# Optimization experiments

Hardware: AMD Instinct MI355X
Metric: run time of the kernel (lower is better)

The kernel has to match this reference:

```python
import jax, jax.numpy as jnp
import numpy as np

B, S, D, H, L = 32, 512, 256, 8, 3
HD = D // H
FFN = D // 2
SCALE_BASE = 512.0
EPS = 1e-5


def _gammas():
    return (1.0 - jnp.exp(jnp.linspace(np.log(1.0 / 32.0), np.log(1.0 / 512.0), H))).astype(jnp.float32)


def _xpos(x, downscale):
    # x: [..., S, hd]; XPOS rotary embedding with exponential length scaling
    s, hd = x.shape[-2], x.shape[-1]
    half = hd // 2
    scale = (jnp.arange(0, hd, 2, dtype=jnp.float32) + 0.4 * hd) / (1.4 * hd)  # [half]
    power = jnp.arange(s, dtype=jnp.float32)[:, None] / SCALE_BASE
    sm = scale[None, :] ** power  # [S, half]
    if downscale:
        sm = 1.0 / sm
    inv_freq = 1.0 / (10000.0 ** (jnp.arange(half, dtype=jnp.float32) / half))
    ang = jnp.arange(s, dtype=jnp.float32)[:, None] * inv_freq[None, :]  # [S, half]
    sin = jnp.repeat(jnp.sin(ang) * sm, 2, axis=-1)  # duplicate_interleave -> [S, hd]
    cos = jnp.repeat(jnp.cos(ang) * sm, 2, axis=-1)
    x1, x2 = x[..., ::2], x[..., 1::2]
    rot = jnp.stack((-x2, x1), axis=-1).reshape(x.shape)  # rotate_every_two
    return x * cos + rot * sin


def _layer_norm(x, w, b):
    mu = x.mean(-1, keepdims=True)
    var = ((x - mu) ** 2).mean(-1, keepdims=True)
    return (x - mu) / jnp.sqrt(var + EPS) * w + b


def _msr(X, WQ, WK, WV, WG, WO, gn_w, gn_b):
    # Multi-scale retention, parallel form. X: [B,S,D]; WQ/WK/WV: [H,D,HD]
    b, s, _ = X.shape
    Q = _xpos(jnp.einsum('bsd,hde->bhse', X, WQ), False)
    K = _xpos(jnp.einsum('bsd,hde->bhse', X, WK), True)
    V = jnp.einsum('bsd,hde->bhse', X, WV)
    n = jnp.arange(s)
    delta = (n[:, None] - n[None, :]).astype(jnp.float32)
    mask = n[:, None] >= n[None, :]
    g = _gammas()
    Dm = jnp.where(mask[None], g[:, None, None] ** delta[None], 0.0)  # [H,S,S]
    scores = jnp.einsum('bhse,bhte->bhst', Q, K) * Dm[None]  # [B,H,S,S]
    Y = jnp.einsum('bhst,bhte->bhse', scores, V)  # [B,H,S,HD]
    Y = jnp.moveaxis(Y, 1, 2)  # [B,S,H,HD] (= concat heads)
    # GroupNorm(heads, v_dim): normalize per (token, head) group
    mu = Y.mean(-1, keepdims=True)
    var = ((Y - mu) ** 2).mean(-1, keepdims=True)
    Yn = ((Y - mu) / jnp.sqrt(var + EPS)).reshape(b, s, D) * gn_w + gn_b
    G = X @ WG
    return (G * jax.nn.sigmoid(G) * Yn) @ WO


def setup_inputs() -> dict:
    key = jax.random.key(0)
    ks = jax.random.split(key, 10)
    inp = {
        'v': jax.random.randint(ks[0], (B, S), 0, 65, dtype=jnp.int64),
        'emb': jax.random.normal(ks[1], (65, D), dtype=jnp.float32),
        'WQ': jax.random.normal(ks[2], (L, H, D, HD), dtype=jnp.float32) / D,
        'WK': jax.random.normal(ks[3], (L, H, D, HD), dtype=jnp.float32) / D,
        'WV': jax.random.normal(ks[4], (L, H, D, HD), dtype=jnp.float32) / D,
        'WG': jax.random.normal(ks[5], (L, D, D), dtype=jnp.float32) / D,
        'WO': jax.random.normal(ks[6], (L, D, D), dtype=jnp.float32) / D,
        'gn_w': jnp.ones((L, D), jnp.float32),
        'gn_b': jnp.zeros((L, D), jnp.float32),
        'ln1_w': jnp.ones((L, D), jnp.float32),
        'ln1_b': jnp.zeros((L, D), jnp.float32),
        'ln2_w': jnp.ones((L, D), jnp.float32),
        'ln2_b': jnp.zeros((L, D), jnp.float32),
        'w1': jax.random.normal(ks[7], (L, D, FFN), dtype=jnp.float32) * (1.0 / np.sqrt(D)),
        'b1': jnp.zeros((L, FFN), jnp.float32),
        'w2': jax.random.normal(ks[8], (L, FFN, D), dtype=jnp.float32) * (1.0 / np.sqrt(FFN)),
        'b2': jnp.zeros((L, D), jnp.float32),
    }
    return inp


def reference(v, emb, WQ, WK, WV, WG, WO, gn_w, gn_b, ln1_w, ln1_b, ln2_w, ln2_b, w1, b1, w2, b2):
    emb = emb.at[0].set(0.0)  # padding_idx=0
    X = jax.nn.relu(emb[v])  # [B,S,D]
    for i in range(L):
        Y = _msr(_layer_norm(X, ln1_w[i], ln1_b[i]), WQ[i], WK[i], WV[i], WG[i], WO[i], gn_w[i], gn_b[i]) + X
        h = jax.nn.gelu(_layer_norm(Y, ln2_w[i], ln2_b[i]) @ w1[i] + b1[i], approximate=False)
        X = h @ w2[i] + b2[i] + Y
    return X
```

## Files before the change

### kernel.cpp

```cpp
#include <hip/hip_runtime.h>
#include <hip/hip_bf16.h>
#include <math.h>

#define BB 32
#define SS 512
#define DD 256
#define HH 8
#define HDIM 32
#define FFNN 128
#define NROWS (BB*SS)
#define NELEM (NROWS*DD)

using bf16 = __hip_bfloat16;
typedef __attribute__((ext_vector_type(8))) short short8;
typedef __attribute__((ext_vector_type(4))) short short4v;
typedef __attribute__((ext_vector_type(4))) float floatx4;
typedef unsigned int uint_al __attribute__((may_alias));

static __device__ __forceinline__ float bf2f(bf16 x) { return __bfloat162float(x); }
static __device__ __forceinline__ bf16  f2bf(float x) { return __float2bfloat16(x); }
static __device__ __forceinline__ short f2bfs(float x) {
    bf16 b = __float2bfloat16(x);
    return __builtin_bit_cast(short, b);
}

static __device__ __forceinline__ unsigned int cvtpk(float a, float b) {
    unsigned int r;
    asm("v_cvt_pk_bf16_f32 %0, %1, %2" : "=v"(r) : "v"(a), "v"(b));
    return r;
}
static __device__ __forceinline__ short4v mk4(unsigned int a, unsigned int b) {
    union { unsigned int u[2]; short4v s; } t;
    t.u[0] = a; t.u[1] = b;
    return t.s;
}
static __device__ __forceinline__ floatx4 mfma16(short4v a, short4v b, floatx4 c) {
#if __has_builtin(__builtin_amdgcn_mfma_f32_16x16x16bf16_1k)
    return __builtin_amdgcn_mfma_f32_16x16x16bf16_1k(a, b, c, 0, 0, 0);
#else
    asm("v_mfma_f32_16x16x16_bf16 %0, %1, %2, %0" : "+v"(c) : "v"(a), "v"(b));
    return c;
#endif
}

static __device__ __forceinline__ void gld_lds16(const void* g, void* l) {
    __builtin_amdgcn_global_load_lds(
        (const __attribute__((address_space(1))) void*)g,
        (__attribute__((address_space(3))) void*)l, 16, 0, 0);
}

__global__ __launch_bounds__(256) void detect_v(const int* __restrict__ v, int* __restrict__ flag) {
    int i = blockIdx.x * 256 + threadIdx.x;
    if (v[2 * i + 1] != 0) atomicOr(flag, 1);
}

#define NQKVG (3*1024*256)
#define NWO   (3*256*256)
#define NW1   (3*128*256)
#define NW2   (3*256*128)
#define NXPT  (512*16)
#define NSETUP (NQKVG+NWO+NW1+NW2+NXPT)
__global__ __launch_bounds__(256) void setup_pack(const float* __restrict__ WQ, const float* __restrict__ WK,
                                                  const float* __restrict__ WV, const float* __restrict__ WG,
                                                  const float* __restrict__ WO, const float* __restrict__ w1,
                                                  const float* __restrict__ w2,
                                                  bf16* __restrict__ dQ, bf16* __restrict__ dO,
                                                  bf16* __restrict__ d1, bf16* __restrict__ d2,
                                                  float4* __restrict__ xpt, int* __restrict__ flag) {
    int idx = blockIdx.x * 256 + threadIdx.x;
    if (idx == 0) *flag = 0;
    if (idx < NQKVG) {
        int k = idx & 255, n = (idx >> 8) & 1023, l = idx >> 18;
        int seg = n >> 8, n8 = n & 255;
        float val;
        if (seg < 3) {
            const float* W = (seg == 0) ? WQ : (seg == 1) ? WK : WV;
            int h = n8 >> 5, e = n8 & 31;
            val = W[(((size_t)l * 8 + h) * 256 + k) * 32 + e];
        } else {
            val = WG[(size_t)l * 65536 + k * 256 + n8];
        }
        dQ[((size_t)l * 1024 + n) * 256 + k] = f2bf(val);
    } else if (idx < NQKVG + NWO) {
        int i = idx - NQKVG;
        int k = i & 255, n = (i >> 8) & 255, l = i >> 16;
        dO[((size_t)l * 256 + n) * 256 + k] = f2bf(WO[(size_t)l * 65536 + k * 256 + n]);
    } else if (idx < NQKVG + NWO + NW1) {
        int i = idx - NQKVG - NWO;
        int k = i & 255, n = (i >> 8) & 127, l = i >> 15;
        d1[((size_t)l * 128 + n) * 256 + k] = f2bf(w1[(size_t)l * 32768 + k * 128 + n]);
    } else if (idx < NQKVG + NWO + NW1 + NW2) {
        int i = idx - NQKVG - NWO - NW1;
        int k = i & 127, n = (i >> 7) & 255, l = i >> 15;
        d2[((size_t)l * 256 + n) * 128 + k] = f2bf(w2[(size_t)l * 32768 + k * 256 + n]);
    } else {
        int i = idx - NQKVG - NWO - NW1 - NW2;
        int jf = i & 15, s = i >> 4;
        float base = (2.0f * jf + 12.8f) / 44.8f;
        float sm = powf(base, (float)s * (1.0f / 512.0f));
        float ang = (float)s * powf(10000.0f, -(float)jf / 16.0f);
        float sn, cs;
        sincosf(ang, &sn, &cs);
        xpt[i] = float4{cs * sm, sn * sm, cs / sm, sn / sm};
    }
}

__global__ __launch_bounds__(256) void embed_ln_kernel(const int* __restrict__ v,
                                                       const float* __restrict__ emb,
                                                       const int* __restrict__ flag,
                                                       const float* __restrict__ w,
                                                       const float* __restrict__ b,
                                                       float* __restrict__ X,
                                                       short* __restrict__ Xn) {
    __shared__ float p1[4], p2[4], st[2];
    const int d = threadIdx.x;
    const int wid = threadIdx.x >> 6;
    const int is32 = *flag;
    const float wd = w[d], bd = b[d];
    for (int it = 0; it < 8; ++it) {
        int row = blockIdx.x * 8 + it;
        int tok = is32 ? v[row] : v[2 * row];
        float x = 0.0f;
        if (tok != 0) {
            x = emb[tok * DD + d];
            x = x > 0.0f ? x : 0.0f;
        }
        X[(size_t)row * DD + d] = x;
        float s1 = x, s2 = x * x;
        #pragma unroll
        for (int off = 1; off < 64; off <<= 1) {
            s1 += __shfl_xor(s1, off);
            s2 += __shfl_xor(s2, off);
        }
        if ((threadIdx.x & 63) == 0) { p1[wid] = s1; p2[wid] = s2; }
        __syncthreads();
        if (threadIdx.x == 0) {
            float t1 = p1[0] + p1[1] + p1[2] + p1[3];
            float t2 = p2[0] + p2[1] + p2[2] + p2[3];
            float mu = t1 * (1.0f / DD);
            float var = t2 * (1.0f / DD) - mu * mu;
            st[0] = mu; st[1] = rsqrtf(var + 1e-5f);
        }
        __syncthreads();
        Xn[(size_t)row * DD + d] = f2bfs((x - st[0]) * st[1] * wd + bd);
    }
}

__global__ __launch_bounds__(256) void qkvg_gemm(const short* __restrict__ A,
                                                 const short* __restrict__ Bp,
                                                 const float4* __restrict__ xpt,
                                                 bf16* __restrict__ C) {
    __shared__ __align__(16) short Als[16 * 512];
    __shared__ __align__(16) short Bls[16 * 512];
    const int tid = threadIdx.x;
    const int wave = tid >> 6, lane = tid & 63, lo = lane & 15, quad = lane >> 4;
    const int wm = wave >> 1, wn = wave & 1;
    const int row0 = blockIdx.x * 128, col0 = blockIdx.y * 128;

    floatx4 acc[4][4];
    #pragma unroll
    for (int i = 0; i < 4; ++i)
        #pragma unroll
        for (int j = 0; j < 4; ++j) acc[i][j] = floatx4{0.f, 0.f, 0.f, 0.f};

    for (int k0 = 0; k0 < 256; k0 += 64) {
        #pragma unroll
        for (int t = 0; t < 4; ++t) {
            int grp = (wm * 4 + t) * 2 + wn;
            const short* ga = A + (size_t)(row0 + (wm * 4 + t) * 16 + lo) * 256
                            + k0 + (wn * 4 + quad) * 8;
            gld_lds16(ga, &Als[grp * 512]);
        }
        #pragma unroll
        for (int t = 0; t < 4; ++t) {
            int grp = (wn * 4 + t) * 2 + wm;
            const short* gb = Bp + (size_t)(col0 + (wn * 4 + t) * 16 + lo) * 256
                            + k0 + (wm * 4 + quad) * 8;
            gld_lds16(gb, &Bls[grp * 512]);
        }
        __syncthreads();
        #pragma unroll
        for (int kkgrp = 0; kkgrp < 2; ++kkgrp) {
            short8 af[4], bfr[4];
            #pragma unroll
            for (int t = 0; t < 4; ++t)
                af[t] = *(const short8*)(&Als[((wm * 4 + t) * 2 + kkgrp) * 512 + lane * 8]);
            #pragma unroll
            for (int t = 0; t < 4; ++t)
                bfr[t] = *(const short8*)(&Bls[((wn * 4 + t) * 2 + kkgrp) * 512 + lane * 8]);
            #pragma unroll
            for (int ti = 0; ti < 4; ++ti)
                #pragma unroll
                for (int tj = 0; tj < 4; ++tj)
                    acc[ti][tj] = __builtin_amdgcn_mfma_f32_16x16x32_bf16(af[ti], bfr[tj], acc[ti][tj], 0, 0, 0);
        }
        __syncthreads();
    }

    #pragma unroll
    for (int ti = 0; ti < 4; ++ti) {
        #pragma unroll
        for (int tj = 0; tj < 4; ++tj) {
            int colb = col0 + (wn * 4 + tj) * 16 + lo;
            int seg = colb >> 8;
            #pragma unroll
            for (int r = 0; r < 4; ++r) {
                int row = row0 + (wm * 4 + ti) * 16 + quad * 4 + r;
                float v = acc[ti][tj][r];
                if (seg < 2) {
                    int s = row & (SS - 1);
                    int jf = (colb & 31) >> 1;
                    float4 t = xpt[s * 16 + jf];
                    float cs = (seg == 0) ? t.x : t.z;
                    float sn = (seg == 0) ? t.y : t.w;
                    float p = __shfl_xor(v, 1);
                    v = (lo & 1) ? (v * cs + p * sn) : (v * cs - p * sn);
                }
                C[(size_t)row * 1024 + colb] = f2bf(v);
            }
        }
    }
}

#define HS2 264
#define HSTR 136
template<int DOLN>
__global__ __launch_bounds__(256) void wo_ffn_fused(const short* __restrict__ A,
                                                    const short* __restrict__ Wo,
                                                    const short* __restrict__ W1p,
                                                    const float* __restrict__ b1,
                                                    const short* __restrict__ W2p,
                                                    const float* __restrict__ b2,
                                                    float* __restrict__ X,
                                                    const float* __restrict__ ln2w,
                                                    const float* __restrict__ ln2b,
                                                    const float* __restrict__ ln1w,
                                                    const float* __restrict__ ln1b,
                                                    short* __restrict__ Xn) {
    __shared__ __align__(16) short Hn[32 * HS2];
    __shared__ __align__(16) short Hf[32 * HSTR];
    __shared__ float Ssum[32][4], Ssq[32][4];
    const int tid = threadIdx.x;
    const int wave = tid >> 6, lane = tid & 63, lo = lane & 15, quad = lane >> 4;
    const int row0 = blockIdx.x * 32;
    const int colw0 = wave * 64;
    const int kq = quad * 8;

    floatx4 acc[2][4];
    #pragma unroll
    for (int i = 0; i < 2; ++i)
        #pragma unroll
        for (int j = 0; j < 4; ++j) acc[i][j] = floatx4{0.f, 0.f, 0.f, 0.f};

    for (int k0 = 0; k0 < 256; k0 += 64) {
        #pragma unroll
        for (int kk = 0; kk < 2; ++kk) {
            const int kof = k0 + kk * 32 + kq;
            short8 af[2], bfr[4];
            #pragma unroll
            for (int t = 0; t < 2; ++t)
                af[t] = *(const short8*)(A + (size_t)(row0 + t * 16 + lo) * 1024 + kof);
            #pragma unroll
            for (int t = 0; t < 4; ++t)
                bfr[t] = *(const short8*)(Wo + (size_t)(colw0 + t * 16 + lo) * 256 + kof);
            #pragma unroll
            for (int ti = 0; ti < 2; ++ti)
                #pragma unroll
                for (int tj = 0; tj < 4; ++tj)
                    acc[ti][tj] = __builtin_amdgcn_mfma_f32_16x16x32_bf16(af[ti], bfr[tj], acc[ti][tj], 0, 0, 0);
        }
    }

    float vv[2][4][4];
    #pragma unroll
    for (int ti = 0; ti < 2; ++ti)
        #pragma unroll
        for (int tj = 0; tj < 4; ++tj) {
            int colb = colw0 + tj * 16 + lo;
            #pragma unroll
            for (int r = 0; r < 4; ++r) {
                int row = row0 + ti * 16 + quad * 4 + r;
                vv[ti][tj][r] = acc[ti][tj][r] + X[(size_t)row * DD + colb];
            }
        }
    #pragma unroll
    for (int ti = 0; ti < 2; ++ti)
        #pragma unroll
        for (int r = 0; r < 4; ++r) {
            float s1 = 0.f, s2 = 0.f;
            #pragma unroll
            for (int tj = 0; tj < 4; ++tj) {
                float v = vv[ti][tj][r];
                s1 += v; s2 += v * v;
            }
            #pragma unroll
            for (int off = 1; off < 16; off <<= 1) {
                s1 += __shfl_xor(s1, off);
                s2 += __shfl_xor(s2, off);
            }
            if (lo == 0) {
                int rl = ti * 16 + quad * 4 + r;
                Ssum[rl][wave] = s1;
                Ssq[rl][wave] = s2;
            }
        }
    __syncthreads();
    #pragma unroll
    for (int ti = 0; ti < 2; ++ti)
        #pragma unroll
        for (int r = 0; r < 4; ++r) {
            int rl = ti * 16 + quad * 4 + r;
            float t1 = Ssum[rl][0] + Ssum[rl][1] + Ssum[rl][2] + Ssum[rl][3];
            float t2 = Ssq[rl][0] + Ssq[rl][1] + Ssq[rl][2] + Ssq[rl][3];
            float mu = t1 * (1.0f / DD);
            float var = t2 * (1.0f / DD) - mu * mu;
            float rs = rsqrtf(var + 1e-5f);
            #pragma unroll
            for (int tj = 0; tj < 4; ++tj) {
                int colb = colw0 + tj * 16 + lo;
                Hn[rl * HS2 + colb] =
                    f2bfs((vv[ti][tj][r] - mu) * rs * ln2w[colb] + ln2b[colb]);
            }
        }
    __syncthreads();

    floatx4 a1[2][2];
    #pragma unroll
    for (int i = 0; i < 2; ++i) { a1[i][0] = floatx4{0,0,0,0}; a1[i][1] = floatx4{0,0,0,0}; }
    for (int k0 = 0; k0 < 256; k0 += 64) {
        #pragma unroll
        for (int kk = 0; kk < 2; ++kk) {
            const int kof = k0 + kk * 32 + kq;
            short8 af[2], bfr[2];
            #pragma unroll
            for (int t = 0; t < 2; ++t)
                af[t] = *(const short8*)(&Hn[(t * 16 + lo) * HS2 + kof]);
            #pragma unroll
            for (int t = 0; t < 2; ++t)
                bfr[t] = *(const short8*)(W1p + (size_t)(wave * 32 + t * 16 + lo) * 256 + kof);
            #pragma unroll
            for (int ti = 0; ti < 2; ++ti)
                #pragma unroll
                for (int tj = 0; tj < 2; ++tj)
                    a1[ti][tj] = __builtin_amdgcn_mfma_f32_16x16x32_bf16(af[ti], bfr[tj], a1[ti][tj], 0, 0, 0);
        }
    }
    #pragma unroll
    for (int ti = 0; ti < 2; ++ti)
        #pragma unroll
        for (int tj = 0; tj < 2; ++tj) {
            int colb = wave * 32 + tj * 16 + lo;
            float bs = b1[colb];
            #pragma unroll
            for (int r = 0; r < 4; ++r) {
                int rl = ti * 16 + quad * 4 + r;
                float v = a1[ti][tj][r] + bs;
                v = 0.5f * v * (1.0f + erff(v * 0.70710678118f));
                Hf[rl * HSTR + colb] = f2bfs(v);
            }
        }
    __syncthreads();

    floatx4 a2[2][4];
    #pragma unroll
    for (int i = 0; i < 2; ++i)
        #pragma unroll
        for (int j = 0; j < 4; ++j) a2[i][j] = floatx4{0,0,0,0};
    for (int k0 = 0; k0 < 128; k0 += 64) {
        #pragma unroll
        for (int kk = 0; kk < 2; ++kk) {
            const int kof = k0 + kk * 32 + kq;
            short8 af[2], bfr[4];
            #pragma unroll
            for (int t = 0; t < 2; ++t)
                af[t] = *(const short8*)(&Hf[(t * 16 + lo) * HSTR + kof]);
            #pragma unroll
            for (int t = 0; t < 4; ++t)
                bfr[t] = *(const short8*)(W2p + (size_t)(colw0 + t * 16 + lo) * 128 + kof);
            #pragma unroll
            for (int ti = 0; ti < 2; ++ti)
                #pragma unroll
                for (int tj = 0; tj < 4; ++tj)
                    a2[ti][tj] = __builtin_amdgcn_mfma_f32_16x16x32_bf16(af[ti], bfr[tj], a2[ti][tj], 0, 0, 0);
        }
    }

    #pragma unroll
    for (int ti = 0; ti < 2; ++ti)
        #pragma unroll
        for (int tj = 0; tj < 4; ++tj) {
            int colb = colw0 + tj * 16 + lo;
            float bs = b2[colb];
            #pragma unroll
            for (int r = 0; r < 4; ++r) {
                int row = row0 + ti * 16 + quad * 4 + r;
                float v = a2[ti][tj][r] + bs + vv[ti][tj][r];
                X[(size_t)row * DD + colb] = v;
                vv[ti][tj][r] = v;
            }
        }
    if (!DOLN) return;
    #pragma unroll
    for (int ti = 0; ti < 2; ++ti)
        #pragma unroll
        for (int r = 0; r < 4; ++r) {
            float s1 = 0.f, s2 = 0.f;
            #pragma unroll
            for (int tj = 0; tj < 4; ++tj) {
                float v = vv[ti][tj][r];
                s1 += v; s2 += v * v;
            }
            #pragma unroll
            for (int off = 1; off < 16; off <<= 1) {
                s1 += __shfl_xor(s1, off);
                s2 += __shfl_xor(s2, off);
            }
            if (lo == 0) {
                int rl = ti * 16 + quad * 4 + r;
                Ssum[rl][wave] = s1;
                Ssq[rl][wave] = s2;
            }
        }
    __syncthreads();
    #pragma unroll
    for (int ti = 0; ti < 2; ++ti)
        #pragma unroll
        for (int r = 0; r < 4; ++r) {
            int rl = ti * 16 + quad * 4 + r;
            float t1 = Ssum[rl][0] + Ssum[rl][1] + Ssum[rl][2] + Ssum[rl][3];
            float t2 = Ssq[rl][0] + Ssq[rl][1] + Ssq[rl][2] + Ssq[rl][3];
            float mu = t1 * (1.0f / DD);
            float var = t2 * (1.0f / DD) - mu * mu;
            float rs = rsqrtf(var + 1e-5f);
            int row = row0 + rl;
            #pragma unroll
            for (int tj = 0; tj < 4; ++tj) {
                int colb = colw0 + tj * 16 + lo;
                Xn[(size_t)row * DD + colb] =
                    f2bfs((vv[ti][tj][r] - mu) * rs * ln1w[colb] + ln1b[colb]);
            }
        }
}

#define VSTR 44
__global__ __launch_bounds__(256) void retention_mfma_kernel(bf16* __restrict__ QKVG,
                                                             const float* __restrict__ gnw,
                                                             const float* __restrict__ gnb) {
    __shared__ __align__(16) short Vt[4][32 * VSTR];
    const int wslot = threadIdx.x >> 6;
    const int lane = threadIdx.x & 63;
    const int gblk = blockIdx.x >> 6;
    const int qi = 15 - ((gblk & ~3) + (((gblk & 3) + (gblk >> 2)) & 3));
    const int bh = ((blockIdx.x & 63) << 2) | wslot;
    const int b = bh >> 3, h = bh & 7;
    const int q0 = qi * 32;
    const int lo = lane & 15, quad = lane >> 4;

    const float la0 = -3.46573590280f, la1 = -6.23832462504f;
    float gamma = 1.0f - expf(la0 + (float)h * (la1 - la0) / 7.0f);
    float lg2 = log2f(gamma);
    float g16i = exp2f(-16.0f * lg2);
    float g16p = exp2f(16.0f * lg2);
    float gi32 = exp2f(-32.0f * lg2);
    float wq[4], wq16[4], wqB[4];
    #pragma unroll
    for (int r = 0; r < 4; ++r) {
        wq[r]   = exp2f((float)(lo - 4 * quad - r) * lg2);
        wq16[r] = wq[r] * g16i;
        wqB[r]  = wq[r] * g16p;
    }
    float c = exp2f((float)q0 * lg2);

    const size_t base = (size_t)b * SS * 1024;
    const short* QKVGs = (const short*)QKVG;

    short8 qfA = *(const short8*)(QKVGs + base + (size_t)(q0 + lo) * 1024 + h * HDIM + quad * 8);
    short8 qfB = *(const short8*)(QKVGs + base + (size_t)(q0 + 16 + lo) * 1024 + h * HDIM + quad * 8);

    floatx4 oA0 = {0,0,0,0}, oA1 = {0,0,0,0}, oB0 = {0,0,0,0}, oB1 = {0,0,0,0};
    short* Vw = Vt[wslot];
    const int nch = qi + 1;

    for (int ch = 0; ch < nch; ++ch) {
        const int t0 = ch * 32;
        const short* Kb = QKVGs + base + 256 + h * HDIM + quad * 8;
        short8 kf0 = *(const short8*)(Kb + (size_t)(t0 + lo) * 1024);
        short8 kf1 = *(const short8*)(Kb + (size_t)(t0 + 16 + lo) * 1024);
        {
            const int r = lane >> 2, dcol = (lane & 3) * 8;
            const short* Vg = QKVGs + base + 512 + h * HDIM + dcol;
            uint4 u1 = *(const uint4*)(Vg + (size_t)(t0 + r) * 1024);
            uint4 u2 = *(const uint4*)(Vg + (size_t)(t0 + 16 + r) * 1024);
            uint_al* W1 = (uint_al*)(Vw + r * VSTR + dcol);
            uint_al* W2 = (uint_al*)(Vw + (16 + r) * VSTR + dcol);
            W1[0] = u1.x; W1[1] = u1.y; W1[2] = u1.z; W1[3] = u1.w;
            W2[0] = u2.x; W2[1] = u2.y; W2[2] = u2.z; W2[3] = u2.w;
        }
        const floatx4 z = {0,0,0,0};
        __builtin_amdgcn_s_setprio(1);
        floatx4 sA0 = __builtin_amdgcn_mfma_f32_16x16x32_bf16(kf0, qfA, z, 0, 0, 0);
        floatx4 sA1 = __builtin_amdgcn_mfma_f32_16x16x32_bf16(kf1, qfA, z, 0, 0, 0);
        floatx4 sB0 = __builtin_amdgcn_mfma_f32_16x16x32_bf16(kf0, qfB, z, 0, 0, 0);
        floatx4 sB1 = __builtin_amdgcn_mfma_f32_16x16x32_bf16(kf1, qfB, z, 0, 0, 0);
        __builtin_amdgcn_s_setprio(0);

        float m0[4], m1[4], mB[4];
        #pragma unroll
        for (int r = 0; r < 4; ++r) {
            m0[r] = c * wq[r];
            m1[r] = c * wq16[r];
            mB[r] = c * wqB[r];
        }
        if (ch == qi) {
            #pragma unroll
            for (int r = 0; r < 4; ++r) {
                if (lo < 4 * quad + r) m0[r] = 0.0f;
                m1[r] = 0.0f;
            }
        }
        c *= gi32;

        unsigned int pa0 = cvtpk(sA0[0] * m0[0], sA0[1] * m0[1]);
        unsigned int pa1 = cvtpk(sA0[2] * m0[2], sA0[3] * m0[3]);
        unsigned int pa2 = cvtpk(sA1[0] * m1[0], sA1[1] * m1[1]);
        unsigned int pa3 = cvtpk(sA1[2] * m1[2], sA1[3] * m1[3]);
        unsigned int pb0 = cvtpk(sB0[0] * mB[0], sB0[1] * mB[1]);
        unsigned int pb1 = cvtpk(sB0[2] * mB[2], sB0[3] * mB[3]);
        unsigned int pb2 = cvtpk(sB1[0] * m0[0], sB1[1] * m0[1]);
        unsigned int pb3 = cvtpk(sB1[2] * m0[2], sB1[3] * m0[3]);
        short4v pA0 = mk4(pa0, pa1), pA1 = mk4(pa2, pa3);
        short4v pB0 = mk4(pb0, pb1), pB1 = mk4(pb2, pb3);

        short4v v00, v01, v10, v11;
        #pragma unroll
        for (int j = 0; j < 4; ++j) {
            v00[j] = Vw[(4 * quad + j) * VSTR + lo];
            v01[j] = Vw[(16 + 4 * quad + j) * VSTR + lo];
            v10[j] = Vw[(4 * quad + j) * VSTR + 16 + lo];
            v11[j] = Vw[(16 + 4 * quad + j) * VSTR + 16 + lo];
        }
        __builtin_amdgcn_s_setprio(1);
        oA0 = mfma16(pA0, v00, oA0);
        oA0 = mfma16(pA1, v01, oA0);
        oA1 = mfma16(pA0, v10, oA1);
        oA1 = mfma16(pA1, v11, oA1);
        oB0 = mfma16(pB0, v00, oB0);
        oB0 = mfma16(pB1, v01, oB0);
        oB1 = mfma16(pB0, v10, oB1);
        oB1 = mfma16(pB1, v11, oB1);
        __builtin_amdgcn_s_setprio(0);
    }

    float gw0 = gnw[h * HDIM + lo], gw1 = gnw[h * HDIM + 16 + lo];
    float gb0 = gnb[h * HDIM + lo], gb1 = gnb[h * HDIM + 16 + lo];
    bf16* QK = QKVG;
    #pragma unroll
    for (int sub = 0; sub < 2; ++sub) {
        floatx4 o0 = sub ? oB0 : oA0;
        floatx4 o1 = sub ? oB1 : oA1;
        int qbase = q0 + sub * 16;
        #pragma unroll
        for (int r = 0; r < 4; ++r) {
            float y0 = o0[r], y1 = o1[r];
            float s = y0 + y1, ss = y0 * y0 + y1 * y1;
            #pragma unroll
            for (int off = 1; off < 16; off <<= 1) {
                s  += __shfl_xor(s, off);
                ss += __shfl_xor(ss, off);
            }
            float mu = s * (1.0f / HDIM);
            float var = ss * (1.0f / HDIM) - mu * mu;
            float rstd = rsqrtf(var + 1e-5f);
            int q = qbase + quad * 4 + r;
            size_t rowb = base + (size_t)q * 1024;
            float g0 = bf2f(QK[rowb + 768 + h * HDIM + lo]);
            float g1 = bf2f(QK[rowb + 768 + h * HDIM + 16 + lo]);
            float t0v = g0 / (1.0f + expf(-g0)) * ((y0 - mu) * rstd * gw0 + gb0);
            float t1v = g1 / (1.0f + expf(-g1)) * ((y1 - mu) * rstd * gw1 + gb1);
            QK[rowb + h * HDIM + lo]      = f2bf(t0v);
            QK[rowb + h * HDIM + 16 + lo] = f2bf(t1v);
        }
    }
}

extern "C" void kernel_launch(void* const* d_in, const int* in_sizes, int n_in,
                              void* d_out, int out_size, void* d_ws, size_t ws_size,
                              hipStream_t stream) {
    const int*   v    = (const int*)d_in[0];
    const float* emb  = (const float*)d_in[1];
    const float* WQ   = (const float*)d_in[2];
    const float* WK   = (const float*)d_in[3];
    const float* WV   = (const float*)d_in[4];
    const float* WG   = (const float*)d_in[5];
    const float* WO   = (const float*)d_in[6];
    const float* gn_w = (const float*)d_in[7];
    const float* gn_b = (const float*)d_in[8];
    const float* ln1w = (const float*)d_in[9];
    const float* ln1b = (const float*)d_in[10];
    const float* ln2w = (const float*)d_in[11];
    const float* ln2b = (const float*)d_in[12];
    const float* w1   = (const float*)d_in[13];
    const float* b1   = (const float*)d_in[14];
    const float* w2   = (const float*)d_in[15];
    const float* b2   = (const float*)d_in[16];

    float* X = (float*)d_out;

    float* base  = (float*)d_ws;
    int*   flag  = (int*)base;
    short* Xn    = (short*)(base + 16);
    bf16*  QKVG  = (bf16*)(Xn + (size_t)NROWS * 256);
    bf16*  WqkvgP = QKVG + (size_t)NROWS * 1024;
    bf16*  WoP   = WqkvgP + 3 * 1024 * 256;
    bf16*  W1P   = WoP + 3 * 256 * 256;
    bf16*  W2P   = W1P + 3 * 128 * 256;
    float4* xpt  = (float4*)(W2P + 3 * 256 * 128);

    setup_pack<<<NSETUP / 256, 256, 0, stream>>>(WQ, WK, WV, WG, WO, w1, w2,
                                                 WqkvgP, WoP, W1P, W2P, xpt, flag);
    detect_v<<<32, 256, 0, stream>>>(v, flag);
    embed_ln_kernel<<<NROWS / 8, 256, 0, stream>>>(v, emb, flag, ln1w, ln1b, X, Xn);

    for (int i = 0; i < 3; ++i) {
        qkvg_gemm<<<dim3(128, 8), 256, 0, stream>>>(Xn,
                                                    (const short*)(WqkvgP + (size_t)i * 1024 * 256),
                                                    xpt, QKVG);
        retention_mfma_kernel<<<1024, 256, 0, stream>>>(QKVG, gn_w + i * DD, gn_b + i * DD);
        if (i < 2)
            wo_ffn_fused<1><<<NROWS / 32, 256, 0, stream>>>((const short*)QKVG,
                                                            (const short*)(WoP + (size_t)i * 256 * 256),
                                                            (const short*)(W1P + (size_t)i * 128 * 256),
                                                            b1 + i * FFNN,
                                                            (const short*)(W2P + (size_t)i * 256 * 128),
                                                            b2 + i * DD, X,
                                                            ln2w + i * DD, ln2b + i * DD,
                                                            ln1w + (i + 1) * DD, ln1b + (i + 1) * DD, Xn);
        else
            wo_ffn_fused<0><<<NROWS / 32, 256, 0, stream>>>((const short*)QKVG,
                                                            (const short*)(WoP + (size_t)i * 256 * 256),
                                                            (const short*)(W1P + (size_t)i * 128 * 256),
                                                            b1 + i * FFNN,
                                                            (const short*)(W2P + (size_t)i * 256 * 128),
                                                            b2 + i * DD, X,
                                                            ln2w + i * DD, ln2b + i * DD,
                                                            nullptr, nullptr, nullptr);
    }
}
```

Before: 352.1 us.

## Fuse retention into the Wo/FFN kernel with one wave per head

Merges the retention kernel into the output-projection and FFN kernel. Each 512-thread block now owns one 32-row query chunk of one batch, with eight waves each computing one head. The gated, group-normed retention output goes straight into shared memory as the Wo GEMM input, so it is no longer written back to QKVG and re-read, and one launch per layer disappears. The costs are a causally imbalanced workload per block: blocks with later query chunks do more retention work, only partly offset by alternating the chunk order across block indices. There are also only 512 blocks, which lowers parallelism, and the GEMM phases are split into narrower per-wave column slices.

```diff
diff --git a/kernel.cpp b/kernel.cpp
--- a/kernel.cpp
+++ b/kernel.cpp
@@ -222,240 +222,40 @@
     }
 }
 
-#define HS2 264
+#define TSTR 264
 #define HSTR 136
+#define VSTR 44
 template<int DOLN>
-__global__ __launch_bounds__(256) void wo_ffn_fused(const short* __restrict__ A,
-                                                    const short* __restrict__ Wo,
-                                                    const short* __restrict__ W1p,
-                                                    const float* __restrict__ b1,
-                                                    const short* __restrict__ W2p,
-                                                    const float* __restrict__ b2,
-                                                    float* __restrict__ X,
-                                                    const float* __restrict__ ln2w,
-                                                    const float* __restrict__ ln2b,
-                                                    const float* __restrict__ ln1w,
-                                                    const float* __restrict__ ln1b,
-                                                    short* __restrict__ Xn) {
-    __shared__ __align__(16) short Hn[32 * HS2];
+__global__ __launch_bounds__(512) void ret_wo_ffn(const bf16* __restrict__ QKVG,
+                                                  const float* __restrict__ gnw,
+                                                  const float* __restrict__ gnb,
+                                                  const short* __restrict__ Wo,
+                                                  const short* __restrict__ W1p,
+                                                  const float* __restrict__ b1,
+                                                  const short* __restrict__ W2p,
+                                                  const float* __restrict__ b2,
+                                                  float* __restrict__ X,
+                                                  const float* __restrict__ ln2w,
+                                                  const float* __restrict__ ln2b,
+                                                  const float* __restrict__ ln1w,
+                                                  const float* __restrict__ ln1b,
+                                                  short* __restrict__ Xn) {
+    __shared__ __align__(16) short Vt[8][32 * VSTR];
+    __shared__ __align__(16) short Tn[32 * TSTR];
     __shared__ __align__(16) short Hf[32 * HSTR];
-    __shared__ float Ssum[32][4], Ssq[32][4];
+    __shared__ float Ssum[32][8], Ssq[32][8];
     const int tid = threadIdx.x;
     const int wave = tid >> 6, lane = tid & 63, lo = lane & 15, quad = lane >> 4;
-    const int row0 = blockIdx.x * 32;
-    const int colw0 = wave * 64;
+    const int blk = blockIdx.x;
+    const int qi = (blk < 256) ? (blk & 15) : 15 - (blk & 15);
+    const int bb = (blk & 255) >> 4 | ((blk >> 4) & 16);
+    const int q0 = qi * 32;
+    const int row0 = bb * SS + q0;
+    const int h = wave;
     const int kq = quad * 8;
 
-    floatx4 acc[2][4];
-    #pragma unroll
-    for (int i = 0; i < 2; ++i)
-        #pragma unroll
-        for (int j = 0; j < 4; ++j) acc[i][j] = floatx4{0.f, 0.f, 0.f, 0.f};
-
-    for (int k0 = 0; k0 < 256; k0 += 64) {
-        #pragma unroll
-        for (int kk = 0; kk < 2; ++kk) {
-            const int kof = k0 + kk * 32 + kq;
-            short8 af[2], bfr[4];
-            #pragma unroll
-            for (int t = 0; t < 2; ++t)
-                af[t] = *(const short8*)(A + (size_t)(row0 + t * 16 + lo) * 1024 + kof);
-            #pragma unroll
-            for (int t = 0; t < 4; ++t)
-                bfr[t] = *(const short8*)(Wo + (size_t)(colw0 + t * 16 + lo) * 256 + kof);
-            #pragma unroll
-            for (int ti = 0; ti < 2; ++ti)
-                #pragma unroll
-                for (int tj = 0; tj < 4; ++tj)
-                    acc[ti][tj] = __builtin_amdgcn_mfma_f32_16x16x32_bf16(af[ti], bfr[tj], acc[ti][tj], 0, 0, 0);
-        }
-    }
-
-    float vv[2][4][4];
-    #pragma unroll
-    for (int ti = 0; ti < 2; ++ti)
-        #pragma unroll
-        for (int tj = 0; tj < 4; ++tj) {
-            int colb = colw0 + tj * 16 + lo;
-            #pragma unroll
-            for (int r = 0; r < 4; ++r) {
-                int row = row0 + ti * 16 + quad * 4 + r;
-                vv[ti][tj][r] = acc[ti][tj][r] + X[(size_t)row * DD + colb];
-            }
-        }
-    #pragma unroll
-    for (int ti = 0; ti < 2; ++ti)
-        #pragma unroll
-        for (int r = 0; r < 4; ++r) {
-            float s1 = 0.f, s2 = 0.f;
-            #pragma unroll
-            for (int tj = 0; tj < 4; ++tj) {
-                float v = vv[ti][tj][r];
-                s1 += v; s2 += v * v;
-            }
-            #pragma unroll
-            for (int off = 1; off < 16; off <<= 1) {
-                s1 += __shfl_xor(s1, off);
-                s2 += __shfl_xor(s2, off);
-            }
-            if (lo == 0) {
-                int rl = ti * 16 + quad * 4 + r;
-                Ssum[rl][wave] = s1;
-                Ssq[rl][wave] = s2;
-            }
-        }
-    __syncthreads();
-    #pragma unroll
-    for (int ti = 0; ti < 2; ++ti)
-        #pragma unroll
-        for (int r = 0; r < 4; ++r) {
-            int rl = ti * 16 + quad * 4 + r;
-            float t1 = Ssum[rl][0] + Ssum[rl][1] + Ssum[rl][2] + Ssum[rl][3];
-            float t2 = Ssq[rl][0] + Ssq[rl][1] + Ssq[rl][2] + Ssq[rl][3];
-            float mu = t1 * (1.0f / DD);
-            float var = t2 * (1.0f / DD) - mu * mu;
-            float rs = rsqrtf(var + 1e-5f);
-            #pragma unroll
-            for (int tj = 0; tj < 4; ++tj) {
-                int colb = colw0 + tj * 16 + lo;
-                Hn[rl * HS2 + colb] =
-                    f2bfs((vv[ti][tj][r] - mu) * rs * ln2w[colb] + ln2b[colb]);
-            }
-        }
-    __syncthreads();
-
-    floatx4 a1[2][2];
-    #pragma unroll
-    for (int i = 0; i < 2; ++i) { a1[i][0] = floatx4{0,0,0,0}; a1[i][1] = floatx4{0,0,0,0}; }
-    for (int k0 = 0; k0 < 256; k0 += 64) {
-        #pragma unroll
-        for (int kk = 0; kk < 2; ++kk) {
-            const int kof = k0 + kk * 32 + kq;
-            short8 af[2], bfr[2];
-            #pragma unroll
-            for (int t = 0; t < 2; ++t)
-                af[t] = *(const short8*)(&Hn[(t * 16 + lo) * HS2 + kof]);
-            #pragma unroll
-            for (int t = 0; t < 2; ++t)
-                bfr[t] = *(const short8*)(W1p + (size_t)(wave * 32 + t * 16 + lo) * 256 + kof);
-            #pragma unroll
-            for (int ti = 0; ti < 2; ++ti)
-                #pragma unroll
-                for (int tj = 0; tj < 2; ++tj)
-                    a1[ti][tj] = __builtin_amdgcn_mfma_f32_16x16x32_bf16(af[ti], bfr[tj], a1[ti][tj], 0, 0, 0);
-        }
-    }
-    #pragma unroll
-    for (int ti = 0; ti < 2; ++ti)
-        #pragma unroll
-        for (int tj = 0; tj < 2; ++tj) {
-            int colb = wave * 32 + tj * 16 + lo;
-            float bs = b1[colb];
-            #pragma unroll
-            for (int r = 0; r < 4; ++r) {
-                int rl = ti * 16 + quad * 4 + r;
-                float v = a1[ti][tj][r] + bs;
-                v = 0.5f * v * (1.0f + erff(v * 0.70710678118f));
-                Hf[rl * HSTR + colb] = f2bfs(v);
-            }
-        }
-    __syncthreads();
-
-    floatx4 a2[2][4];
-    #pragma unroll
-    for (int i = 0; i < 2; ++i)
-        #pragma unroll
-        for (int j = 0; j < 4; ++j) a2[i][j] = floatx4{0,0,0,0};
-    for (int k0 = 0; k0 < 128; k0 += 64) {
-        #pragma unroll
-        for (int kk = 0; kk < 2; ++kk) {
-            const int kof = k0 + kk * 32 + kq;
-            short8 af[2], bfr[4];
-            #pragma unroll
-            for (int t = 0; t < 2; ++t)
-                af[t] = *(const short8*)(&Hf[(t * 16 + lo) * HSTR + kof]);
-            #pragma unroll
-            for (int t = 0; t < 4; ++t)
-                bfr[t] = *(const short8*)(W2p + (size_t)(colw0 + t * 16 + lo) * 128 + kof);
-            #pragma unroll
-            for (int ti = 0; ti < 2; ++ti)
-                #pragma unroll
-                for (int tj = 0; tj < 4; ++tj)
-                    a2[ti][tj] = __builtin_amdgcn_mfma_f32_16x16x32_bf16(af[ti], bfr[tj], a2[ti][tj], 0, 0, 0);
-        }
-    }
-
-    #pragma unroll
-    for (int ti = 0; ti < 2; ++ti)
-        #pragma unroll
-        for (int tj = 0; tj < 4; ++tj) {
-            int colb = colw0 + tj * 16 + lo;
-            float bs = b2[colb];
-            #pragma unroll
-            for (int r = 0; r < 4; ++r) {
-                int row = row0 + ti * 16 + quad * 4 + r;
-                float v = a2[ti][tj][r] + bs + vv[ti][tj][r];
-                X[(size_t)row * DD + colb] = v;
-                vv[ti][tj][r] = v;
-            }
-        }
-    if (!DOLN) return;
-    #pragma unroll
-    for (int ti = 0; ti < 2; ++ti)
-        #pragma unroll
-        for (int r = 0; r < 4; ++r) {
-            float s1 = 0.f, s2 = 0.f;
-            #pragma unroll
-            for (int tj = 0; tj < 4; ++tj) {
-                float v = vv[ti][tj][r];
-                s1 += v; s2 += v * v;
-            }
-            #pragma unroll
-            for (int off = 1; off < 16; off <<= 1) {
-                s1 += __shfl_xor(s1, off);
-                s2 += __shfl_xor(s2, off);
-            }
-            if (lo == 0) {
-                int rl = ti * 16 + quad * 4 + r;
-                Ssum[rl][wave] = s1;
-                Ssq[rl][wave] = s2;
-            }
-        }
-    __syncthreads();
-    #pragma unroll
-    for (int ti = 0; ti < 2; ++ti)
-        #pragma unroll
-        for (int r = 0; r < 4; ++r) {
-            int rl = ti * 16 + quad * 4 + r;
-            float t1 = Ssum[rl][0] + Ssum[rl][1] + Ssum[rl][2] + Ssum[rl][3];
-            float t2 = Ssq[rl][0] + Ssq[rl][1] + Ssq[rl][2] + Ssq[rl][3];
-            float mu = t1 * (1.0f / DD);
-            float var = t2 * (1.0f / DD) - mu * mu;
-            float rs = rsqrtf(var + 1e-5f);
-            int row = row0 + rl;
-            #pragma unroll
-            for (int tj = 0; tj < 4; ++tj) {
-                int colb = colw0 + tj * 16 + lo;
-                Xn[(size_t)row * DD + colb] =
-                    f2bfs((vv[ti][tj][r] - mu) * rs * ln1w[colb] + ln1b[colb]);
-            }
-        }
-}
-
-#define VSTR 44
-__global__ __launch_bounds__(256) void retention_mfma_kernel(bf16* __restrict__ QKVG,
-                                                             const float* __restrict__ gnw,
-                                                             const float* __restrict__ gnb) {
-    __shared__ __align__(16) short Vt[4][32 * VSTR];
-    const int wslot = threadIdx.x >> 6;
-    const int lane = threadIdx.x & 63;
-    const int gblk = blockIdx.x >> 6;
-    const int qi = 15 - ((gblk & ~3) + (((gblk & 3) + (gblk >> 2)) & 3));
-    const int bh = ((blockIdx.x & 63) << 2) | wslot;
-    const int b = bh >> 3, h = bh & 7;
-    const int q0 = qi * 32;
-    const int lo = lane & 15, quad = lane >> 4;
-
+    const size_t base = (size_t)bb * SS * 1024;
+    const short* QKVGs = (const short*)QKVG;
     const float la0 = -3.46573590280f, la1 = -6.23832462504f;
     float gamma = 1.0f - expf(la0 + (float)h * (la1 - la0) / 7.0f);
     float lg2 = log2f(gamma);
@@ -471,28 +271,25 @@
     }
     float c = exp2f((float)q0 * lg2);
 
-    const size_t base = (size_t)b * SS * 1024;
-    const short* QKVGs = (const short*)QKVG;
-
-    short8 qfA = *(const short8*)(QKVGs + base + (size_t)(q0 + lo) * 1024 + h * HDIM + quad * 8);
-    short8 qfB = *(const short8*)(QKVGs + base + (size_t)(q0 + 16 + lo) * 1024 + h * HDIM + quad * 8);
+    short8 qfA = *(const short8*)(QKVGs + base + (size_t)(q0 + lo) * 1024 + h * HDIM + kq);
+    short8 qfB = *(const short8*)(QKVGs + base + (size_t)(q0 + 16 + lo) * 1024 + h * HDIM + kq);
 
     floatx4 oA0 = {0,0,0,0}, oA1 = {0,0,0,0}, oB0 = {0,0,0,0}, oB1 = {0,0,0,0};
-    short* Vw = Vt[wslot];
+    short* Vw = Vt[wave];
     const int nch = qi + 1;
 
     for (int ch = 0; ch < nch; ++ch) {
         const int t0 = ch * 32;
-        const short* Kb = QKVGs + base + 256 + h * HDIM + quad * 8;
+        const short* Kb = QKVGs + base + 256 + h * HDIM + kq;
         short8 kf0 = *(const short8*)(Kb + (size_t)(t0 + lo) * 1024);
         short8 kf1 = *(const short8*)(Kb + (size_t)(t0 + 16 + lo) * 1024);
         {
-            const int r = lane >> 2, dcol = (lane & 3) * 8;
+            const int vr = lane >> 2, dcol = (lane & 3) * 8;
             const short* Vg = QKVGs + base + 512 + h * HDIM + dcol;
-            uint4 u1 = *(const uint4*)(Vg + (size_t)(t0 + r) * 1024);
-            uint4 u2 = *(const uint4*)(Vg + (size_t)(t0 + 16 + r) * 1024);
-            uint_al* W1 = (uint_al*)(Vw + r * VSTR + dcol);
-            uint_al* W2 = (uint_al*)(Vw + (16 + r) * VSTR + dcol);
+            uint4 u1 = *(const uint4*)(Vg + (size_t)(t0 + vr) * 1024);
+            uint4 u2 = *(const uint4*)(Vg + (size_t)(t0 + 16 + vr) * 1024);
+            uint_al* W1 = (uint_al*)(Vw + vr * VSTR + dcol);
+            uint_al* W2 = (uint_al*)(Vw + (16 + vr) * VSTR + dcol);
             W1[0] = u1.x; W1[1] = u1.y; W1[2] = u1.z; W1[3] = u1.w;
             W2[0] = u2.x; W2[1] = u2.y; W2[2] = u2.z; W2[3] = u2.w;
         }
@@ -551,36 +348,223 @@
         __builtin_amdgcn_s_setprio(0);
     }
 
-    float gw0 = gnw[h * HDIM + lo], gw1 = gnw[h * HDIM + 16 + lo];
-    float gb0 = gnb[h * HDIM + lo], gb1 = gnb[h * HDIM + 16 + lo];
-    bf16* QK = QKVG;
-    #pragma unroll
-    for (int sub = 0; sub < 2; ++sub) {
-        floatx4 o0 = sub ? oB0 : oA0;
-        floatx4 o1 = sub ? oB1 : oA1;
-        int qbase = q0 + sub * 16;
+    {
+        float gw0 = gnw[h * HDIM + lo], gw1 = gnw[h * HDIM + 16 + lo];
+        float gb0 = gnb[h * HDIM + lo], gb1 = gnb[h * HDIM + 16 + lo];
+        #pragma unroll
+        for (int sub = 0; sub < 2; ++sub) {
+            floatx4 o0 = sub ? oB0 : oA0;
+            floatx4 o1 = sub ? oB1 : oA1;
+            #pragma unroll
+            for (int r = 0; r < 4; ++r) {
+                float y0 = o0[r], y1 = o1[r];
+                float s = y0 + y1, ss = y0 * y0 + y1 * y1;
+                #pragma unroll
+                for (int off = 1; off < 16; off <<= 1) {
+                    s  += __shfl_xor(s, off);
+                    ss += __shfl_xor(ss, off);
+                }
+                float mu = s * (1.0f / HDIM);
+                float var = ss * (1.0f / HDIM) - mu * mu;
+                float rstd = rsqrtf(var + 1e-5f);
+                int rl = sub * 16 + quad * 4 + r;
+                size_t rowb = base + (size_t)(q0 + rl) * 1024;
+                float g0 = bf2f(QKVG[rowb + 768 + h * HDIM + lo]);
+                float g1 = bf2f(QKVG[rowb + 768 + h * HDIM + 16 + lo]);
+                float t0v = g0 / (1.0f + expf(-g0)) * ((y0 - mu) * rstd * gw0 + gb0);
+                float t1v = g1 / (1.0f + expf(-g1)) * ((y1 - mu) * rstd * gw1 + gb1);
+                Tn[rl * TSTR + h * HDIM + lo]      = f2bfs(t0v);
+                Tn[rl * TSTR + h * HDIM + 16 + lo] = f2bfs(t1v);
+            }
+        }
+    }
+    __syncthreads();
+
+    floatx4 acc[2][2];
+    #pragma unroll
+    for (int i = 0; i < 2; ++i) { acc[i][0] = floatx4{0,0,0,0}; acc[i][1] = floatx4{0,0,0,0}; }
+    for (int k0 = 0; k0 < 256; k0 += 64) {
+        #pragma unroll
+        for (int kk = 0; kk < 2; ++kk) {
+            const int kof = k0 + kk * 32 + kq;
+            short8 af[2], bfr[2];
+            #pragma unroll
+            for (int t = 0; t < 2; ++t)
+                af[t] = *(const short8*)(&Tn[(t * 16 + lo) * TSTR + kof]);
+            #pragma unroll
+            for (int t = 0; t < 2; ++t)
+                bfr[t] = *(const short8*)(Wo + (size_t)(wave * 32 + t * 16 + lo) * 256 + kof);
+            #pragma unroll
+            for (int ti = 0; ti < 2; ++ti)
+                #pragma unroll
+                for (int tj = 0; tj < 2; ++tj)
+                    acc[ti][tj] = __builtin_amdgcn_mfma_f32_16x16x32_bf16(af[ti], bfr[tj], acc[ti][tj], 0, 0, 0);
+        }
+    }
+
+    float vv[2][2][4];
+    #pragma unroll
+    for (int ti = 0; ti < 2; ++ti)
+        #pragma unroll
+        for (int tj = 0; tj < 2; ++tj) {
+            int colb = wave * 32 + tj * 16 + lo;
+            #pragma unroll
+            for (int r = 0; r < 4; ++r) {
+                int row = row0 + ti * 16 + quad * 4 + r;
+                vv[ti][tj][r] = acc[ti][tj][r] + X[(size_t)row * DD + colb];
+            }
+        }
+    #pragma unroll
+    for (int ti = 0; ti < 2; ++ti)
         #pragma unroll
         for (int r = 0; r < 4; ++r) {
-            float y0 = o0[r], y1 = o1[r];
-            float s = y0 + y1, ss = y0 * y0 + y1 * y1;
+            float s1 = 0.f, s2 = 0.f;
+            #pragma unroll
+            for (int tj = 0; tj < 2; ++tj) {
+                float v = vv[ti][tj][r];
+                s1 += v; s2 += v * v;
+            }
             #pragma unroll
             for (int off = 1; off < 16; off <<= 1) {
-                s  += __shfl_xor(s, off);
-                ss += __shfl_xor(ss, off);
-            }
-            float mu = s * (1.0f / HDIM);
-            float var = ss * (1.0f / HDIM) - mu * mu;
-            float rstd = rsqrtf(var + 1e-5f);
-            int q = qbase + quad * 4 + r;
-            size_t rowb = base + (size_t)q * 1024;
-            float g0 = bf2f(QK[rowb + 768 + h * HDIM + lo]);
-            float g1 = bf2f(QK[rowb + 768 + h * HDIM + 16 + lo]);
-            float t0v = g0 / (1.0f + expf(-g0)) * ((y0 - mu) * rstd * gw0 + gb0);
-            float t1v = g1 / (1.0f + expf(-g1)) * ((y1 - mu) * rstd * gw1 + gb1);
-            QK[rowb + h * HDIM + lo]      = f2bf(t0v);
-            QK[rowb + h * HDIM + 16 + lo] = f2bf(t1v);
-        }
-    }
+                s1 += __shfl_xor(s1, off);
+                s2 += __shfl_xor(s2, off);
+            }
+            if (lo == 0) {
+                int rl = ti * 16 + quad * 4 + r;
+                Ssum[rl][wave] = s1;
+                Ssq[rl][wave] = s2;
+            }
+        }
+    __syncthreads();
+    #pragma unroll
+    for (int ti = 0; ti < 2; ++ti)
+        #pragma unroll
+        for (int r = 0; r < 4; ++r) {
+            int rl = ti * 16 + quad * 4 + r;
+            float t1 = 0.f, t2 = 0.f;
+            #pragma unroll
+            for (int w8 = 0; w8 < 8; ++w8) { t1 += Ssum[rl][w8]; t2 += Ssq[rl][w8]; }
+            float mu = t1 * (1.0f / DD);
+            float var = t2 * (1.0f / DD) - mu * mu;
+            float rs = rsqrtf(var + 1e-5f);
+            #pragma unroll
+            for (int tj = 0; tj < 2; ++tj) {
+                int colb = wave * 32 + tj * 16 + lo;
+                Tn[rl * TSTR + colb] =
+                    f2bfs((vv[ti][tj][r] - mu) * rs * ln2w[colb] + ln2b[colb]);
+            }
+        }
+    __syncthreads();
+
+    floatx4 a1[2];
+    a1[0] = floatx4{0,0,0,0}; a1[1] = floatx4{0,0,0,0};
+    for (int k0 = 0; k0 < 256; k0 += 64) {
+        #pragma unroll
+        for (int kk = 0; kk < 2; ++kk) {
+            const int kof = k0 + kk * 32 + kq;
+            short8 af[2], bfr;
+            #pragma unroll
+            for (int t = 0; t < 2; ++t)
+                af[t] = *(const short8*)(&Tn[(t * 16 + lo) * TSTR + kof]);
+            bfr = *(const short8*)(W1p + (size_t)(wave * 16 + lo) * 256 + kof);
+            #pragma unroll
+            for (int ti = 0; ti < 2; ++ti)
+                a1[ti] = __builtin_amdgcn_mfma_f32_16x16x32_bf16(af[ti], bfr, a1[ti], 0, 0, 0);
+        }
+    }
+    {
+        int colb = wave * 16 + lo;
+        float bs = b1[colb];
+        #pragma unroll
+        for (int ti = 0; ti < 2; ++ti)
+            #pragma unroll
+            for (int r = 0; r < 4; ++r) {
+                int rl = ti * 16 + quad * 4 + r;
+                float v = a1[ti][r] + bs;
+                v = 0.5f * v * (1.0f + erff(v * 0.70710678118f));
+                Hf[rl * HSTR + colb] = f2bfs(v);
+            }
+    }
+    __syncthreads();
+
+    floatx4 a2[2][2];
+    #pragma unroll
+    for (int i = 0; i < 2; ++i) { a2[i][0] = floatx4{0,0,0,0}; a2[i][1] = floatx4{0,0,0,0}; }
+    for (int k0 = 0; k0 < 128; k0 += 64) {
+        #pragma unroll
+        for (int kk = 0; kk < 2; ++kk) {
+            const int kof = k0 + kk * 32 + kq;
+            short8 af[2], bfr[2];
+            #pragma unroll
+            for (int t = 0; t < 2; ++t)
+                af[t] = *(const short8*)(&Hf[(t * 16 + lo) * HSTR + kof]);
+            #pragma unroll
+            for (int t = 0; t < 2; ++t)
+                bfr[t] = *(const short8*)(W2p + (size_t)(wave * 32 + t * 16 + lo) * 128 + kof);
+            #pragma unroll
+            for (int ti = 0; ti < 2; ++ti)
+                #pragma unroll
+                for (int tj = 0; tj < 2; ++tj)
+                    a2[ti][tj] = __builtin_amdgcn_mfma_f32_16x16x32_bf16(af[ti], bfr[tj], a2[ti][tj], 0, 0, 0);
+        }
+    }
+
+    #pragma unroll
+    for (int ti = 0; ti < 2; ++ti)
+        #pragma unroll
+        for (int tj = 0; tj < 2; ++tj) {
+            int colb = wave * 32 + tj * 16 + lo;
+            float bs = b2[colb];
+            #pragma unroll
+            for (int r = 0; r < 4; ++r) {
+                int row = row0 + ti * 16 + quad * 4 + r;
+                float v = a2[ti][tj][r] + bs + vv[ti][tj][r];
+                X[(size_t)row * DD + colb] = v;
+                vv[ti][tj][r] = v;
+            }
+        }
+    if (!DOLN) return;
+    #pragma unroll
+    for (int ti = 0; ti < 2; ++ti)
+        #pragma unroll
+        for (int r = 0; r < 4; ++r) {
+            float s1 = 0.f, s2 = 0.f;
+            #pragma unroll
+            for (int tj = 0; tj < 2; ++tj) {
+                float v = vv[ti][tj][r];
+                s1 += v; s2 += v * v;
+            }
+            #pragma unroll
+            for (int off = 1; off < 16; off <<= 1) {
+                s1 += __shfl_xor(s1, off);
+                s2 += __shfl_xor(s2, off);
+            }
+            if (lo == 0) {
+                int rl = ti * 16 + quad * 4 + r;
+                Ssum[rl][wave] = s1;
+                Ssq[rl][wave] = s2;
+            }
+        }
+    __syncthreads();
+    #pragma unroll
+    for (int ti = 0; ti < 2; ++ti)
+        #pragma unroll
+        for (int r = 0; r < 4; ++r) {
+            int rl = ti * 16 + quad * 4 + r;
+            float t1 = 0.f, t2 = 0.f;
+            #pragma unroll
+            for (int w8 = 0; w8 < 8; ++w8) { t1 += Ssum[rl][w8]; t2 += Ssq[rl][w8]; }
+            float mu = t1 * (1.0f / DD);
+            float var = t2 * (1.0f / DD) - mu * mu;
+            float rs = rsqrtf(var + 1e-5f);
+            int row = row0 + rl;
+            #pragma unroll
+            for (int tj = 0; tj < 2; ++tj) {
+                int colb = wave * 32 + tj * 16 + lo;
+                Xn[(size_t)row * DD + colb] =
+                    f2bfs((vv[ti][tj][r] - mu) * rs * ln1w[colb] + ln1b[colb]);
+            }
+        }
 }
 
 extern "C" void kernel_launch(void* const* d_in, const int* in_sizes, int n_in,
@@ -625,24 +609,23 @@
         qkvg_gemm<<<dim3(128, 8), 256, 0, stream>>>(Xn,
                                                     (const short*)(WqkvgP + (size_t)i * 1024 * 256),
                                                     xpt, QKVG);
-        retention_mfma_kernel<<<1024, 256, 0, stream>>>(QKVG, gn_w + i * DD, gn_b + i * DD);
         if (i < 2)
-            wo_ffn_fused<1><<<NROWS / 32, 256, 0, stream>>>((const short*)QKVG,
-                                                            (const short*)(WoP + (size_t)i * 256 * 256),
-                                                            (const short*)(W1P + (size_t)i * 128 * 256),
-                                                            b1 + i * FFNN,
-                                                            (const short*)(W2P + (size_t)i * 256 * 128),
-                                                            b2 + i * DD, X,
-                                                            ln2w + i * DD, ln2b + i * DD,
-                                                            ln1w + (i + 1) * DD, ln1b + (i + 1) * DD, Xn);
+            ret_wo_ffn<1><<<512, 512, 0, stream>>>(QKVG, gn_w + i * DD, gn_b + i * DD,
+                                                   (const short*)(WoP + (size_t)i * 256 * 256),
+                                                   (const short*)(W1P + (size_t)i * 128 * 256),
+                                                   b1 + i * FFNN,
+                                                   (const short*)(W2P + (size_t)i * 256 * 128),
+                                                   b2 + i * DD, X,
+                                                   ln2w + i * DD, ln2b + i * DD,
+                                                   ln1w + (i + 1) * DD, ln1b + (i + 1) * DD, Xn);
         else
-            wo_ffn_fused<0><<<NROWS / 32, 256, 0, stream>>>((const short*)QKVG,
-                                                            (const short*)(WoP + (size_t)i * 256 * 256),
-                                                            (const short*)(W1P + (size_t)i * 128 * 256),
-                                                            b1 + i * FFNN,
-                                                            (const short*)(W2P + (size_t)i * 256 * 128),
-                                                            b2 + i * DD, X,
-                                                            ln2w + i * DD, ln2b + i * DD,
-                                                            nullptr, nullptr, nullptr);
-    }
-}
+            ret_wo_ffn<0><<<512, 512, 0, stream>>>(QKVG, gn_w + i * DD, gn_b + i * DD,
+                                                   (const short*)(WoP + (size_t)i * 256 * 256),
+                                                   (const short*)(W1P + (size_t)i * 128 * 256),
+                                                   b1 + i * FFNN,
+                                                   (const short*)(W2P + (size_t)i * 256 * 128),
+                                                   b2 + i * DD, X,
+                                                   ln2w + i * DD, ln2b + i * DD,
+                                                   nullptr, nullptr, nullptr);
+    }
+}
```

Result: no change. 353.2 us (+0.3%).
